# Kernel tuning notes

Hardware: AMD Instinct MI355X
Metric: run time of the kernel (lower is better)

The kernel has to match this reference:

```python
import jax, jax.numpy as jnp
import numpy as np

B, P, D, T = 4096, 19000, 4000, 32
H1, H2 = 2048, 1024
DIN = 2 * P + 2


def setup_inputs() -> dict:
    key = jax.random.key(0)
    ks = jax.random.split(key, 9)
    drug_pairs = jax.random.randint(ks[0], (B, 2), 0, D)
    drug_targets = jax.random.randint(ks[1], (D, T), 0, P)
    conc = jax.random.uniform(ks[2], (B, 2), dtype=jnp.float32)
    s = lambda n: 1.0 / np.sqrt(n).astype(np.float32)
    W1 = jax.random.normal(ks[3], (DIN, H1), dtype=jnp.float32) * s(DIN)
    b1 = jnp.zeros((H1,), jnp.float32)
    W2 = jax.random.normal(ks[4], (H1, H2), dtype=jnp.float32) * s(H1)
    b2 = jnp.zeros((H2,), jnp.float32)
    W3 = jax.random.normal(ks[5], (H2, 1), dtype=jnp.float32) * s(H2)
    b3 = jnp.zeros((1,), jnp.float32)
    return {"drug_pairs": drug_pairs, "drug_targets": drug_targets, "conc": conc,
            "W1": W1, "b1": b1, "W2": W2, "b2": b2, "W3": W3, "b3": b3}


def _multi_hot(drug_ids, drug_targets):
    # drug_ids: [B]; gather per-drug target lists [B, T], scatter 1s into [B, P]
    tgt = drug_targets[drug_ids]  # [B, T]
    rows = jnp.arange(drug_ids.shape[0])[:, None]
    return jnp.zeros((drug_ids.shape[0], P), jnp.float32).at[rows, tgt].set(1.0)


def reference(drug_pairs, drug_targets, conc, W1, b1, W2, b2, W3, b3):
    prot_1 = _multi_hot(drug_pairs[:, 0], drug_targets)  # [B, P]
    prot_2 = _multi_hot(drug_pairs[:, 1], drug_targets)  # [B, P]
    data_1 = jnp.concatenate([prot_1, conc[:, 0:1]], axis=1)  # [B, P+1]
    data_2 = jnp.concatenate([prot_2, conc[:, 1:2]], axis=1)
    order_1 = jnp.concatenate([data_1, data_2], axis=1)  # [B, 2P+2]
    order_2 = jnp.concatenate([data_2, data_1], axis=1)

    def mlp(x):
        h = jax.nn.relu(x @ W1 + b1)
        h = jax.nn.relu(h @ W2 + b2)
        return h @ W3 + b3

    return (mlp(order_1)[:, 0], mlp(order_2)[:, 0])
```

## Files before the change

kernel.cpp:

```cpp
#include <hip/hip_runtime.h>
#include <stdint.h>

#define B_N  4096
#define P_N  19000
#define D_N  4000
#define T_N  32
#define H1_N 2048
#define H2_N 1024

typedef __bf16 bf16x8 __attribute__((ext_vector_type(8)));
typedef float  f32x4  __attribute__((ext_vector_type(4)));

__device__ __forceinline__ unsigned short f2bf(float f) {
  union { float f; uint32_t u; } v; v.f = f;
  uint32_t u = v.u;
  uint32_t r = (u + 0x7fffu + ((u >> 16) & 1u)) >> 16;
  return (unsigned short)r;
}

__device__ __forceinline__ float bflo(uint32_t u) {
  union { uint32_t u; float f; } v; v.u = u << 16; return v.f;
}
__device__ __forceinline__ float bfhi(uint32_t u) {
  union { uint32_t u; float f; } v; v.u = u & 0xffff0000u; return v.f;
}

__device__ __forceinline__ void gload16(const void* g, void* l) {
  __builtin_amdgcn_global_load_lds((const __attribute__((address_space(1))) void*)g,
                                   (__attribute__((address_space(3))) void*)l,
                                   16, 0, 0);
}

__global__ __launch_bounds__(256) void k_conv(const float* __restrict__ W1,
                                              unsigned short* __restrict__ W1b) {
  const size_t base = (size_t)blockIdx.x * H1_N + threadIdx.x * 8;
  const float4* p = (const float4*)(W1 + base);
  float4 x = p[0], y = p[1];
  unsigned short r[8] = { f2bf(x.x), f2bf(x.y), f2bf(x.z), f2bf(x.w),
                          f2bf(y.x), f2bf(y.y), f2bf(y.z), f2bf(y.w) };
  *(uint4*)(W1b + base) = *(uint4*)r;
}

__global__ __launch_bounds__(256) void k_dsum(const int* __restrict__ dt,
                                              const unsigned short* __restrict__ W1b,
                                              float* __restrict__ SA, float* __restrict__ SB) {
  __shared__ int   tgt[T_N];
  __shared__ float wgt[T_N];
  const int d   = blockIdx.x;
  const int tid = threadIdx.x;
  if (tid < T_N) tgt[tid] = dt[d * T_N + tid];
  __syncthreads();
  if (tid < T_N) {
    int v = 1, t = tgt[tid];
    for (int j = 0; j < tid; ++j) v &= (tgt[j] != t);
    wgt[tid] = (float)v;
  }
  __syncthreads();
  const int c0 = tid * 8;
  float aA[8] = {0,0,0,0,0,0,0,0};
  float aB[8] = {0,0,0,0,0,0,0,0};
  #pragma unroll 4
  for (int t = 0; t < T_N; ++t) {
    const float  w   = wgt[t];
    const size_t row = (size_t)tgt[t];
    uint4 a = *(const uint4*)(W1b + row * H1_N + c0);
    uint4 b = *(const uint4*)(W1b + (19001 + row) * H1_N + c0);
    uint32_t au[4] = {a.x, a.y, a.z, a.w};
    uint32_t bu[4] = {b.x, b.y, b.z, b.w};
    #pragma unroll
    for (int k = 0; k < 4; ++k) {
      aA[2*k]   = fmaf(w, bflo(au[k]), aA[2*k]);
      aA[2*k+1] = fmaf(w, bfhi(au[k]), aA[2*k+1]);
      aB[2*k]   = fmaf(w, bflo(bu[k]), aB[2*k]);
      aB[2*k+1] = fmaf(w, bfhi(bu[k]), aB[2*k+1]);
    }
  }
  float4 o;
  o.x=aA[0]; o.y=aA[1]; o.z=aA[2]; o.w=aA[3];
  *(float4*)(SA + (size_t)d * H1_N + c0)     = o;
  o.x=aA[4]; o.y=aA[5]; o.z=aA[6]; o.w=aA[7];
  *(float4*)(SA + (size_t)d * H1_N + c0 + 4) = o;
  o.x=aB[0]; o.y=aB[1]; o.z=aB[2]; o.w=aB[3];
  *(float4*)(SB + (size_t)d * H1_N + c0)     = o;
  o.x=aB[4]; o.y=aB[5]; o.z=aB[6]; o.w=aB[7];
  *(float4*)(SB + (size_t)d * H1_N + c0 + 4) = o;
}

__global__ __launch_bounds__(256) void k_w2t(const float* __restrict__ W2, unsigned short* __restrict__ W2T) {
  __shared__ float tile[32][33];
  const int bx = blockIdx.x & 31;
  const int by = blockIdx.x >> 5;
  const int tx = threadIdx.x & 31, ty = threadIdx.x >> 5;
  #pragma unroll
  for (int i = 0; i < 4; ++i)
    tile[ty + i*8][tx] = W2[(size_t)(by*32 + ty + i*8) * H2_N + bx*32 + tx];
  __syncthreads();
  #pragma unroll
  for (int i = 0; i < 4; ++i) {
    const int n = bx*32 + ty + i*8;
    const int k = by*32 + tx;
    W2T[(size_t)n * H1_N + k] = f2bf(tile[tx][ty + i*8]);
  }
}

__global__ __launch_bounds__(256) void k_h1(const int* __restrict__ dp, const float* __restrict__ conc,
                                            const float* __restrict__ W1, const float* __restrict__ b1,
                                            const float* __restrict__ SA, const float* __restrict__ SB,
                                            unsigned short* __restrict__ h1) {
  const int rI   = blockIdx.x;
  const int swap = (rI >= B_N) ? 1 : 0;
  const int rr   = swap ? rI - B_N : rI;
  const int dA = dp[2*rr + swap];
  const int dB = dp[2*rr + (1 - swap)];
  const float cA = conc[2*rr + swap];
  const float cB = conc[2*rr + (1 - swap)];
  const int c0 = threadIdx.x * 8;
  const float4* sa = (const float4*)(SA + (size_t)dA * H1_N + c0);
  const float4* sb = (const float4*)(SB + (size_t)dB * H1_N + c0);
  const float4* wp = (const float4*)(W1 + (size_t)P_N * H1_N + c0);
  const float4* wq = (const float4*)(W1 + (size_t)(2*P_N + 1) * H1_N + c0);
  const float4* bp = (const float4*)(b1 + c0);
  unsigned short res[8];
  #pragma unroll
  for (int v = 0; v < 2; ++v) {
    float4 a = sa[v], b = sb[v], p = wp[v], q = wq[v], z = bp[v];
    res[v*4+0] = f2bf(fmaxf(a.x + b.x + cA*p.x + cB*q.x + z.x, 0.f));
    res[v*4+1] = f2bf(fmaxf(a.y + b.y + cA*p.y + cB*q.y + z.y, 0.f));
    res[v*4+2] = f2bf(fmaxf(a.z + b.z + cA*p.z + cB*q.z + z.z, 0.f));
    res[v*4+3] = f2bf(fmaxf(a.w + b.w + cA*p.w + cB*q.w + z.w, 0.f));
  }
  *(uint4*)(h1 + (size_t)rI * H1_N + c0) = *(uint4*)res;
}

__global__ __launch_bounds__(256) void k_gemm(const unsigned short* __restrict__ A,
                                              const unsigned short* __restrict__ Bm,
                                              const float* __restrict__ b2,
                                              float* __restrict__ C) {
  __shared__ unsigned short As[128 * 64];
  __shared__ unsigned short Bs[128 * 64];
  const int tid  = threadIdx.x;
  const int wv   = tid >> 6;
  const int lane = tid & 63;
  const int m0 = (blockIdx.x >> 3) * 128;
  const int n0 = (blockIdx.x & 7) * 128;
  const int wm = (wv >> 1) * 64;
  const int wn = (wv & 1) * 64;
  const int r = lane & 15;
  const int g = lane >> 4;
  const int srow = lane >> 3;
  const int slot = (lane & 7) ^ srow;

  f32x4 acc[4][4] = {};

  for (int kt = 0; kt < H1_N / 64; ++kt) {
    const int k0 = kt * 64;
    #pragma unroll
    for (int i = 0; i < 4; ++i) {
      const int c   = i * 4 + wv;
      const int row = c * 8 + srow;
      gload16(A  + (size_t)(m0 + row) * H1_N + k0 + slot * 8, (char*)As + c * 1024);
      gload16(Bm + (size_t)(n0 + row) * H1_N + k0 + slot * 8, (char*)Bs + c * 1024);
    }
    __syncthreads();
    #pragma unroll
    for (int kk = 0; kk < 2; ++kk) {
      bf16x8 af[4], bfr[4];
      #pragma unroll
      for (int mi = 0; mi < 4; ++mi) {
        const int row = wm + mi * 16 + r;
        const int s   = (kk * 4 + g) ^ (row & 7);
        af[mi] = *(const bf16x8*)((const char*)As + row * 128 + s * 16);
      }
      #pragma unroll
      for (int ni = 0; ni < 4; ++ni) {
        const int col = wn + ni * 16 + r;
        const int s   = (kk * 4 + g) ^ (col & 7);
        bfr[ni] = *(const bf16x8*)((const char*)Bs + col * 128 + s * 16);
      }
      #pragma unroll
      for (int mi = 0; mi < 4; ++mi)
        #pragma unroll
        for (int ni = 0; ni < 4; ++ni)
          acc[mi][ni] = __builtin_amdgcn_mfma_f32_16x16x32_bf16(af[mi], bfr[ni], acc[mi][ni], 0, 0, 0);
    }
    __syncthreads();
  }
  #pragma unroll
  for (int ni = 0; ni < 4; ++ni) {
    const int col = n0 + wn + ni * 16 + r;
    const float bb = b2[col];
    #pragma unroll
    for (int mi = 0; mi < 4; ++mi)
      #pragma unroll
      for (int q = 0; q < 4; ++q) {
        const int rowg = m0 + wm + mi * 16 + g * 4 + q;
        C[(size_t)rowg * H2_N + col] = fmaxf(acc[mi][ni][q] + bb, 0.f);
      }
  }
}

__global__ __launch_bounds__(256) void k_out(const float* __restrict__ h2, const float* __restrict__ W3,
                                             const float* __restrict__ b3, float* __restrict__ out) {
  const int row  = blockIdx.x * 4 + (threadIdx.x >> 6);
  const int lane = threadIdx.x & 63;
  const float4* hp = (const float4*)(h2 + (size_t)row * H2_N);
  const float4* wp = (const float4*)W3;
  float s = 0.f;
  #pragma unroll
  for (int j = 0; j < 4; ++j) {
    float4 h = hp[j * 64 + lane];
    float4 w = wp[j * 64 + lane];
    s += h.x * w.x + h.y * w.y + h.z * w.z + h.w * w.w;
  }
  #pragma unroll
  for (int o = 32; o > 0; o >>= 1) s += __shfl_down(s, o, 64);
  if (lane == 0) out[row] = s + b3[0];
}

extern "C" void kernel_launch(void* const* d_in, const int* in_sizes, int n_in,
                              void* d_out, int out_size, void* d_ws, size_t ws_size,
                              hipStream_t stream) {
  const int*   dp   = (const int*)d_in[0];
  const int*   dt   = (const int*)d_in[1];
  const float* conc = (const float*)d_in[2];
  const float* W1   = (const float*)d_in[3];
  const float* b1   = (const float*)d_in[4];
  const float* W2   = (const float*)d_in[5];
  const float* b2   = (const float*)d_in[6];
  const float* W3   = (const float*)d_in[7];
  const float* b3   = (const float*)d_in[8];
  float* out = (float*)d_out;

  char* ws = (char*)d_ws;
  unsigned short* W1b = (unsigned short*)ws;
  unsigned short* h1  = (unsigned short*)ws;
  unsigned short* w2t = (unsigned short*)(ws + 33554432);
  float*          h2  = (float*)(ws + 37748736);
  float*          SA  = (float*)(ws + 155656192);
  float*          SB  = (float*)(ws + 188424192);

  k_conv<<<38002,  256, 0, stream>>>(W1, W1b);
  k_dsum<<<D_N,    256, 0, stream>>>(dt, W1b, SA, SB);
  k_w2t <<<2048,   256, 0, stream>>>(W2, w2t);
  k_h1  <<<2*B_N,  256, 0, stream>>>(dp, conc, W1, b1, SA, SB, h1);
  k_gemm<<<512,    256, 0, stream>>>(h1, w2t, b2, h2);
  k_out <<<2048,   256, 0, stream>>>(h2, W3, b3, out);
}
```

Measured before the change: 306.0 us.

## Fuse output layer into GEMM epilogue, skip unused drugs, store sums in bf16

The W3 dot product and ReLU now run inside the layer-2 GEMM epilogue. Each block writes per-row partial sums to a small buffer that a tiny k_fin kernel reduces, so the full fp32 h2 matrix is never written or re-read. A flag kernel marks which drugs actually appear in drug_pairs, and k_dsum skips blocks for unused drugs. The per-drug sums SA/SB are stored in bf16 to halve their traffic, which adds rounding error before the first layer activation.

```diff
diff --git a/kernel.cpp b/kernel.cpp
--- a/kernel.cpp
+++ b/kernel.cpp
@@ -29,6 +29,14 @@
   __builtin_amdgcn_global_load_lds((const __attribute__((address_space(1))) void*)g,
                                    (__attribute__((address_space(3))) void*)l,
                                    16, 0, 0);
+}
+
+__global__ __launch_bounds__(256) void k_setflags(const int* __restrict__ dp,
+                                                  unsigned char* __restrict__ flags) {
+  const int tid = threadIdx.x;
+  for (int i = tid; i < D_N; i += 256) flags[i] = 0;
+  __syncthreads();
+  for (int i = tid; i < 2 * B_N; i += 256) flags[dp[i]] = 1;
 }
 
 __global__ __launch_bounds__(256) void k_conv(const float* __restrict__ W1,
@@ -42,11 +50,14 @@
 }
 
 __global__ __launch_bounds__(256) void k_dsum(const int* __restrict__ dt,
+                                              const unsigned char* __restrict__ flags,
                                               const unsigned short* __restrict__ W1b,
-                                              float* __restrict__ SA, float* __restrict__ SB) {
+                                              unsigned short* __restrict__ SAb,
+                                              unsigned short* __restrict__ SBb) {
+  const int d = blockIdx.x;
+  if (!flags[d]) return;
   __shared__ int   tgt[T_N];
   __shared__ float wgt[T_N];
-  const int d   = blockIdx.x;
   const int tid = threadIdx.x;
   if (tid < T_N) tgt[tid] = dt[d * T_N + tid];
   __syncthreads();
@@ -75,15 +86,11 @@
       aB[2*k+1] = fmaf(w, bfhi(bu[k]), aB[2*k+1]);
     }
   }
-  float4 o;
-  o.x=aA[0]; o.y=aA[1]; o.z=aA[2]; o.w=aA[3];
-  *(float4*)(SA + (size_t)d * H1_N + c0)     = o;
-  o.x=aA[4]; o.y=aA[5]; o.z=aA[6]; o.w=aA[7];
-  *(float4*)(SA + (size_t)d * H1_N + c0 + 4) = o;
-  o.x=aB[0]; o.y=aB[1]; o.z=aB[2]; o.w=aB[3];
-  *(float4*)(SB + (size_t)d * H1_N + c0)     = o;
-  o.x=aB[4]; o.y=aB[5]; o.z=aB[6]; o.w=aB[7];
-  *(float4*)(SB + (size_t)d * H1_N + c0 + 4) = o;
+  unsigned short oa[8], ob[8];
+  #pragma unroll
+  for (int k = 0; k < 8; ++k) { oa[k] = f2bf(aA[k]); ob[k] = f2bf(aB[k]); }
+  *(uint4*)(SAb + (size_t)d * H1_N + c0) = *(uint4*)oa;
+  *(uint4*)(SBb + (size_t)d * H1_N + c0) = *(uint4*)ob;
 }
 
 __global__ __launch_bounds__(256) void k_w2t(const float* __restrict__ W2, unsigned short* __restrict__ W2T) {
@@ -105,7 +112,8 @@
 
 __global__ __launch_bounds__(256) void k_h1(const int* __restrict__ dp, const float* __restrict__ conc,
                                             const float* __restrict__ W1, const float* __restrict__ b1,
-                                            const float* __restrict__ SA, const float* __restrict__ SB,
+                                            const unsigned short* __restrict__ SAb,
+                                            const unsigned short* __restrict__ SBb,
                                             unsigned short* __restrict__ h1) {
   const int rI   = blockIdx.x;
   const int swap = (rI >= B_N) ? 1 : 0;
@@ -115,29 +123,38 @@
   const float cA = conc[2*rr + swap];
   const float cB = conc[2*rr + (1 - swap)];
   const int c0 = threadIdx.x * 8;
-  const float4* sa = (const float4*)(SA + (size_t)dA * H1_N + c0);
-  const float4* sb = (const float4*)(SB + (size_t)dB * H1_N + c0);
+  uint4 ua = *(const uint4*)(SAb + (size_t)dA * H1_N + c0);
+  uint4 ub = *(const uint4*)(SBb + (size_t)dB * H1_N + c0);
+  uint32_t au[4] = {ua.x, ua.y, ua.z, ua.w};
+  uint32_t bu[4] = {ub.x, ub.y, ub.z, ub.w};
   const float4* wp = (const float4*)(W1 + (size_t)P_N * H1_N + c0);
   const float4* wq = (const float4*)(W1 + (size_t)(2*P_N + 1) * H1_N + c0);
   const float4* bp = (const float4*)(b1 + c0);
+  float a[8], b[8], p[8], q[8], z[8];
+  #pragma unroll
+  for (int k = 0; k < 4; ++k) {
+    a[2*k] = bflo(au[k]); a[2*k+1] = bfhi(au[k]);
+    b[2*k] = bflo(bu[k]); b[2*k+1] = bfhi(bu[k]);
+  }
+  float4 p0 = wp[0], p1 = wp[1], q0 = wq[0], q1 = wq[1], z0 = bp[0], z1 = bp[1];
+  p[0]=p0.x;p[1]=p0.y;p[2]=p0.z;p[3]=p0.w;p[4]=p1.x;p[5]=p1.y;p[6]=p1.z;p[7]=p1.w;
+  q[0]=q0.x;q[1]=q0.y;q[2]=q0.z;q[3]=q0.w;q[4]=q1.x;q[5]=q1.y;q[6]=q1.z;q[7]=q1.w;
+  z[0]=z0.x;z[1]=z0.y;z[2]=z0.z;z[3]=z0.w;z[4]=z1.x;z[5]=z1.y;z[6]=z1.z;z[7]=z1.w;
   unsigned short res[8];
   #pragma unroll
-  for (int v = 0; v < 2; ++v) {
-    float4 a = sa[v], b = sb[v], p = wp[v], q = wq[v], z = bp[v];
-    res[v*4+0] = f2bf(fmaxf(a.x + b.x + cA*p.x + cB*q.x + z.x, 0.f));
-    res[v*4+1] = f2bf(fmaxf(a.y + b.y + cA*p.y + cB*q.y + z.y, 0.f));
-    res[v*4+2] = f2bf(fmaxf(a.z + b.z + cA*p.z + cB*q.z + z.z, 0.f));
-    res[v*4+3] = f2bf(fmaxf(a.w + b.w + cA*p.w + cB*q.w + z.w, 0.f));
-  }
+  for (int k = 0; k < 8; ++k)
+    res[k] = f2bf(fmaxf(a[k] + b[k] + cA*p[k] + cB*q[k] + z[k], 0.f));
   *(uint4*)(h1 + (size_t)rI * H1_N + c0) = *(uint4*)res;
 }
 
 __global__ __launch_bounds__(256) void k_gemm(const unsigned short* __restrict__ A,
                                               const unsigned short* __restrict__ Bm,
                                               const float* __restrict__ b2,
-                                              float* __restrict__ C) {
+                                              const float* __restrict__ W3,
+                                              float* __restrict__ partial) {
   __shared__ unsigned short As[128 * 64];
   __shared__ unsigned short Bs[128 * 64];
+  __shared__ float ps[128];
   const int tid  = threadIdx.x;
   const int wv   = tid >> 6;
   const int lane = tid & 63;
@@ -185,36 +202,58 @@
     }
     __syncthreads();
   }
+  float b2v[4], w3v[4];
   #pragma unroll
   for (int ni = 0; ni < 4; ++ni) {
     const int col = n0 + wn + ni * 16 + r;
-    const float bb = b2[col];
-    #pragma unroll
-    for (int mi = 0; mi < 4; ++mi)
-      #pragma unroll
-      for (int q = 0; q < 4; ++q) {
-        const int rowg = m0 + wm + mi * 16 + g * 4 + q;
-        C[(size_t)rowg * H2_N + col] = fmaxf(acc[mi][ni][q] + bb, 0.f);
-      }
-  }
-}
-
-__global__ __launch_bounds__(256) void k_out(const float* __restrict__ h2, const float* __restrict__ W3,
-                                             const float* __restrict__ b3, float* __restrict__ out) {
-  const int row  = blockIdx.x * 4 + (threadIdx.x >> 6);
-  const int lane = threadIdx.x & 63;
-  const float4* hp = (const float4*)(h2 + (size_t)row * H2_N);
-  const float4* wp = (const float4*)W3;
-  float s = 0.f;
-  #pragma unroll
-  for (int j = 0; j < 4; ++j) {
-    float4 h = hp[j * 64 + lane];
-    float4 w = wp[j * 64 + lane];
-    s += h.x * w.x + h.y * w.y + h.z * w.z + h.w * w.w;
-  }
-  #pragma unroll
-  for (int o = 32; o > 0; o >>= 1) s += __shfl_down(s, o, 64);
-  if (lane == 0) out[row] = s + b3[0];
+    b2v[ni] = b2[col];
+    w3v[ni] = W3[col];
+  }
+  float rs[16];
+  #pragma unroll
+  for (int mi = 0; mi < 4; ++mi)
+    #pragma unroll
+    for (int q = 0; q < 4; ++q) {
+      float s = 0.f;
+      #pragma unroll
+      for (int ni = 0; ni < 4; ++ni)
+        s += fmaxf(acc[mi][ni][q] + b2v[ni], 0.f) * w3v[ni];
+      rs[mi*4+q] = s;
+    }
+  #pragma unroll
+  for (int o = 1; o < 16; o <<= 1)
+    #pragma unroll
+    for (int k = 0; k < 16; ++k)
+      rs[k] += __shfl_xor(rs[k], o, 64);
+  if ((wv & 1) == 0) {
+    if (r == 0)
+      #pragma unroll
+      for (int mi = 0; mi < 4; ++mi)
+        #pragma unroll
+        for (int q = 0; q < 4; ++q)
+          ps[wm + mi*16 + g*4 + q] = rs[mi*4+q];
+  }
+  __syncthreads();
+  if ((wv & 1) == 1) {
+    if (r == 0)
+      #pragma unroll
+      for (int mi = 0; mi < 4; ++mi)
+        #pragma unroll
+        for (int q = 0; q < 4; ++q) {
+          const int rw = wm + mi*16 + g*4 + q;
+          partial[(size_t)(blockIdx.x & 7) * (2*B_N) + m0 + rw] = ps[rw] + rs[mi*4+q];
+        }
+  }
+}
+
+__global__ __launch_bounds__(256) void k_fin(const float* __restrict__ partial,
+                                             const float* __restrict__ b3,
+                                             float* __restrict__ out) {
+  const int i = blockIdx.x * 256 + threadIdx.x;
+  float s = b3[0];
+  #pragma unroll
+  for (int j = 0; j < 8; ++j) s += partial[(size_t)j * (2*B_N) + i];
+  out[i] = s;
 }
 
 extern "C" void kernel_launch(void* const* d_in, const int* in_sizes, int n_in,
@@ -232,17 +271,19 @@
   float* out = (float*)d_out;
 
   char* ws = (char*)d_ws;
-  unsigned short* W1b = (unsigned short*)ws;
-  unsigned short* h1  = (unsigned short*)ws;
-  unsigned short* w2t = (unsigned short*)(ws + 33554432);
-  float*          h2  = (float*)(ws + 37748736);
-  float*          SA  = (float*)(ws + 155656192);
-  float*          SB  = (float*)(ws + 188424192);
-
-  k_conv<<<38002,  256, 0, stream>>>(W1, W1b);
-  k_dsum<<<D_N,    256, 0, stream>>>(dt, W1b, SA, SB);
-  k_w2t <<<2048,   256, 0, stream>>>(W2, w2t);
-  k_h1  <<<2*B_N,  256, 0, stream>>>(dp, conc, W1, b1, SA, SB, h1);
-  k_gemm<<<512,    256, 0, stream>>>(h1, w2t, b2, h2);
-  k_out <<<2048,   256, 0, stream>>>(h2, W3, b3, out);
-}
+  unsigned short* W1b   = (unsigned short*)ws;
+  unsigned short* h1    = (unsigned short*)ws;
+  float*          parts = (float*)(ws + 33554432);
+  unsigned short* SAb   = (unsigned short*)(ws + 155656192);
+  unsigned short* SBb   = (unsigned short*)(ws + 172040192);
+  unsigned short* w2t   = (unsigned short*)(ws + 188424192);
+  unsigned char*  flags = (unsigned char*)(ws + 192618496);
+
+  k_setflags<<<1,     256, 0, stream>>>(dp, flags);
+  k_conv    <<<38002, 256, 0, stream>>>(W1, W1b);
+  k_w2t     <<<2048,  256, 0, stream>>>(W2, w2t);
+  k_dsum    <<<D_N,   256, 0, stream>>>(dt, flags, W1b, SAb, SBb);
+  k_h1      <<<2*B_N, 256, 0, stream>>>(dp, conc, W1, b1, SAb, SBb, h1);
+  k_gemm    <<<512,   256, 0, stream>>>(h1, w2t, b2, W3, parts);
+  k_fin     <<<32,    256, 0, stream>>>(parts, b3, out);
+}
```

Result: faster. 274.8 us (-10.2%).
